# Kernel optimization log

Measured on AMD Instinct MI355X. Metric: run time of the kernel, lower is better.

The kernel has to match this reference:

```python
import jax, jax.numpy as jnp
import numpy as np

H_RES, W_RES = 32, 32
DIM = 512
NUM_HEADS = 16
HEAD_DIM = DIM // NUM_HEADS
SCALE = HEAD_DIM ** -0.5
B = 16
N = H_RES * W_RES
TABLE_SIZE = (2 * H_RES - 1) * (2 * W_RES - 1)


def _relative_position_index():
    coords_h = np.arange(H_RES)
    coords_w = np.arange(W_RES)
    coords = np.stack(np.meshgrid(coords_h, coords_w, indexing='ij'))  # [2, H, W]
    coords_flat = coords.reshape(2, -1)  # [2, N]
    rel = coords_flat[:, :, None] - coords_flat[:, None, :]  # [2, N, N]
    rel = rel.transpose(1, 2, 0).astype(np.int64)  # [N, N, 2]
    rel[:, :, 0] += H_RES - 1
    rel[:, :, 1] += W_RES - 1
    rel[:, :, 0] *= 2 * W_RES - 1
    return rel.sum(-1)  # [N, N]


def setup_inputs() -> dict:
    key = jax.random.key(0)
    ks = jax.random.split(key, 6)
    x = jax.random.normal(ks[0], (B, N, DIM), dtype=jnp.float32)
    w_qkv = jax.random.normal(ks[1], (DIM, 3 * DIM), dtype=jnp.float32) * (DIM ** -0.5)
    b_qkv = jnp.zeros((3 * DIM,), dtype=jnp.float32)
    w_proj = jax.random.normal(ks[2], (DIM, DIM), dtype=jnp.float32) * (DIM ** -0.5)
    b_proj = jnp.zeros((DIM,), dtype=jnp.float32)
    bias_table = jax.random.normal(ks[3], (TABLE_SIZE, NUM_HEADS), dtype=jnp.float32) * 0.02
    rel_index = jnp.asarray(_relative_position_index(), dtype=jnp.int32)
    return {"x": x, "w_qkv": w_qkv, "b_qkv": b_qkv, "w_proj": w_proj,
            "b_proj": b_proj, "bias_table": bias_table, "rel_index": rel_index}


def reference(x, w_qkv, b_qkv, w_proj, b_proj, bias_table, rel_index):
    Bq, Nq, C = x.shape
    qkv = x @ w_qkv + b_qkv  # [B, N, 3C]
    qkv = qkv.reshape(Bq, Nq, 3, NUM_HEADS, HEAD_DIM)
    q = qkv[:, :, 0].transpose(0, 2, 1, 3) * SCALE  # [B, nH, N, d]
    k = qkv[:, :, 1].transpose(0, 2, 1, 3)
    v = qkv[:, :, 2].transpose(0, 2, 1, 3)
    attn = jnp.einsum('bhnd,bhmd->bhnm', q, k)  # [B, nH, N, N]
    bias = bias_table[rel_index]  # [N, N, nH]
    attn = attn + bias.transpose(2, 0, 1)[None]  # broadcast over batch
    attn = jax.nn.softmax(attn, axis=-1)
    out = jnp.einsum('bhnm,bhmd->bhnd', attn, v)  # [B, nH, N, d]
    out = out.transpose(0, 2, 1, 3).reshape(Bq, Nq, C)
    return out @ w_proj + b_proj
```

## Files before the change

kernel.cpp:

```cpp
#include <hip/hip_runtime.h>
#include <hip/hip_bf16.h>
#include <cstdint>
#include <cstddef>

typedef _Float16 f16;
typedef __attribute__((ext_vector_type(8))) _Float16 f16x8;
typedef __attribute__((ext_vector_type(4))) _Float16 f16x4v;
typedef __bf16 bf16;
typedef __attribute__((ext_vector_type(4))) float f32x4;
typedef __attribute__((ext_vector_type(16))) float f32x16;

#define LOG2E 1.4426950408889634f
#define QK_SCALE 0.17677669529663687f

__device__ __forceinline__ f32x4 mfma16f(f16x8 a, f16x8 b, f32x4 c) {
  return __builtin_amdgcn_mfma_f32_16x16x32_f16(a, b, c, 0, 0, 0);
}
__device__ __forceinline__ f32x16 mfma32f(f16x8 a, f16x8 b, f32x16 c) {
  return __builtin_amdgcn_mfma_f32_32x32x16_f16(a, b, c, 0, 0, 0);
}
__device__ __forceinline__ float exp2_hw(float x) {
  float r; asm("v_exp_f32 %0, %1" : "=v"(r) : "v"(x)); return r;
}
__device__ __forceinline__ uint32_t cvtpk_f16(float a, float b) {
  uint32_t r; asm("v_cvt_pkrtz_f16_f32 %0, %1, %2" : "=v"(r) : "v"(a), "v"(b)); return r;
}
__device__ __forceinline__ void pl32swap(uint32_t& a, uint32_t& b) {
  asm("v_permlane32_swap_b32 %0, %1" : "+v"(a), "+v"(b));
}
__device__ __forceinline__ float lo16f(uint32_t u) { return __uint_as_float(u << 16); }
__device__ __forceinline__ float hi16f(uint32_t u) { return __uint_as_float(u & 0xFFFF0000u); }

__device__ __forceinline__ void gl16(const f16* g, f16* l) {
  __builtin_amdgcn_global_load_lds(
      (const __attribute__((address_space(1))) void*)g,
      (__attribute__((address_space(3))) void*)l, 16, 0, 0);
}

__device__ __forceinline__ uint32_t packoff(int m, int k) {
  return (((uint32_t)(m >> 7) * 16u + (uint32_t)(k >> 5)) * 8u + (uint32_t)((m >> 4) & 7)) * 512u
       + (uint32_t)((k >> 3) & 3) * 128u + (uint32_t)(m & 15) * 8u + (uint32_t)(k & 7);
}

__global__ __launch_bounds__(256) void prep_kernel(
    const float* __restrict__ x, const float* __restrict__ wqkv, const float* __restrict__ wproj,
    f16* __restrict__ Xp, f16* __restrict__ Wq, f16* __restrict__ Wp)
{
  const int X4 = 16384 * 512 / 4;
  int e = blockIdx.x * 256 + threadIdx.x;
  if (e < X4) {
    int m = e >> 7, k4 = e & 127;
    f32x4 v = *(const f32x4*)(x + (size_t)e * 4);
    f16x4v o;
    #pragma unroll
    for (int j = 0; j < 4; ++j) o[j] = (f16)v[j];
    *(f16x4v*)(Xp + packoff(m, k4 * 4)) = o;
  } else if (e < X4 + 1536 * 512) {
    int e2 = e - X4;
    int n = e2 >> 9, k = e2 & 511;
    Wq[packoff(n, k)] = (f16)wqkv[k * 1536 + n];
  } else {
    int e3 = e - (X4 + 1536 * 512);
    if (e3 < 512 * 512) {
      int n = e3 >> 9, k = e3 & 511;
      Wp[packoff(n, k)] = (f16)wproj[k * 512 + n];
    }
  }
}

__global__ __launch_bounds__(256) void tblT_kernel(
    const float* __restrict__ btab, float* __restrict__ tblT)
{
  int e = blockIdx.x * 256 + threadIdx.x;
  if (e < 3969 * 16) {
    int h = e & 15, i = e >> 4;
    tblT[h * 4000 + i] = btab[e] * LOG2E;
  }
}

__global__ __launch_bounds__(256) void biasC_kernel(
    const float* __restrict__ tblT, bf16* __restrict__ biasC)
{
  int t = blockIdx.x * 256 + threadIdx.x;
  if (t >= 16 * 63 * 64) return;
  int lane = t & 63;
  int sh = t >> 6;
  int s = sh % 63, h = sh / 63;
  int lq = lane & 31, hi5 = lane >> 5;
  const float* row = tblT + h * 4000 + s * 63 + 31 + lq;
  bf16 o[16];
  #pragma unroll
  for (int r = 0; r < 16; ++r) {
    int kx = (r & 3) + 8 * (r >> 2) + 4 * hi5;
    o[r] = (bf16)row[-kx];
  }
  *(uint4*)(biasC + (size_t)t * 16) = *(uint4*)&o[0];
  *(uint4*)(biasC + (size_t)t * 16 + 8) = *(uint4*)&o[8];
}

template<int NB>
__global__ __launch_bounds__(256) void gemm_frag(
    const f16* __restrict__ Ap, const f16* __restrict__ Bp,
    const float* __restrict__ bvec,
    f16* __restrict__ Qp, f16* __restrict__ Kp, f16* __restrict__ Vt,
    float* __restrict__ out)
{
  __shared__ f16 sA[3][4096];
  __shared__ f16 sB[3][4096];
  const int bid = blockIdx.x;
  const int xcd = bid & 7, idx = bid >> 3;
  int mb, nb;
  if (NB == 12) { int q = idx / 12; mb = xcd * 16 + q; nb = idx - q * 12; }
  else          { mb = xcd * 16 + (idx >> 2); nb = idx & 3; }
  const int tid = threadIdx.x, lane = tid & 63, wave = tid >> 6;
  const int l15 = lane & 15, l4 = lane >> 4;
  const int wr = wave >> 1, wc = wave & 1;

  const f16* gA = Ap + (uint32_t)mb * 65536u + (uint32_t)wave * 1024u + (uint32_t)lane * 8u;
  const f16* gB = Bp + (uint32_t)nb * 65536u + (uint32_t)wave * 1024u + (uint32_t)lane * 8u;
  const int wl = wave * 1024;

  gl16(gA,        &sA[0][wl]);
  gl16(gA + 512,  &sA[0][wl + 512]);
  gl16(gB,        &sB[0][wl]);
  gl16(gB + 512,  &sB[0][wl + 512]);
  gl16(gA + 4096, &sA[1][wl]);
  gl16(gA + 4608, &sA[1][wl + 512]);
  gl16(gB + 4096, &sB[1][wl]);
  gl16(gB + 4608, &sB[1][wl + 512]);

  f32x4 acc[4][4];
  #pragma unroll
  for (int i = 0; i < 4; ++i)
    #pragma unroll
    for (int j = 0; j < 4; ++j) acc[i][j] = (f32x4){0.f, 0.f, 0.f, 0.f};

  const uint32_t aoff = (uint32_t)(wr * 4) * 512u + (uint32_t)lane * 8u;
  const uint32_t boff = (uint32_t)(wc * 4) * 512u + (uint32_t)lane * 8u;

  #pragma unroll
  for (int kt = 0; kt < 16; ++kt) {
    const int s2 = (kt + 2) % 3;
    gl16(gA + (kt + 2) * 4096,       &sA[s2][wl]);
    gl16(gA + (kt + 2) * 4096 + 512, &sA[s2][wl + 512]);
    gl16(gB + (kt + 2) * 4096,       &sB[s2][wl]);
    gl16(gB + (kt + 2) * 4096 + 512, &sB[s2][wl + 512]);
    asm volatile("s_waitcnt vmcnt(8)" ::: "memory");
    asm volatile("s_barrier" ::: "memory");
    const int s0 = kt % 3;
    f16x8 af[4], bfr[4];
    #pragma unroll
    for (int f = 0; f < 4; ++f) {
      af[f]  = *(const f16x8*)&sA[s0][aoff + f * 512];
      bfr[f] = *(const f16x8*)&sB[s0][boff + f * 512];
    }
    asm volatile("s_waitcnt lgkmcnt(0)" ::: "memory");
    asm volatile("s_barrier" ::: "memory");
    #pragma unroll
    for (int mf = 0; mf < 4; ++mf)
      #pragma unroll
      for (int nf = 0; nf < 4; ++nf)
        acc[mf][nf] = mfma16f(af[mf], bfr[nf], acc[mf][nf]);
  }
  asm volatile("s_waitcnt vmcnt(0)" ::: "memory");

  #pragma unroll
  for (int mf = 0; mf < 4; ++mf) {
    #pragma unroll
    for (int nf = 0; nf < 4; ++nf) {
      int colb = nb * 128 + wc * 64 + nf * 16 + l15;
      float bb = bvec[colb];
      #pragma unroll
      for (int i = 0; i < 4; ++i) {
        int m = mb * 128 + wr * 64 + mf * 16 + l4 * 4 + i;
        float v = acc[mf][nf][i] + bb;
        if (NB == 4) {
          out[(size_t)m * 512 + colb] = v;
        } else {
          int t = colb >> 9, cc = colb & 511;
          int b = m >> 10, n = m & 1023;
          int hh = cc >> 5, d = cc & 31;
          int bh2 = b * 16 + hh;
          if (t == 0) {
            v *= (QK_SCALE * LOG2E);
            uint32_t off = (((uint32_t)bh2 * 32u + (uint32_t)(n >> 5)) * 2u + (uint32_t)(d >> 4)) * 512u
                         + ((uint32_t)((d >> 3) & 1) * 32u + (uint32_t)(n & 31)) * 8u + (uint32_t)(d & 7);
            Qp[off] = (f16)v;
          } else if (t == 1) {
            Kp[((size_t)(bh2 * 2 + (d >> 4)) * 1024 + n) * 16 + (d & 15)] = (f16)v;
          } else {
            Vt[((size_t)(bh2 * 128 + (n >> 3)) * 32 + d) * 8 + (n & 7)] = (f16)v;
          }
        }
      }
    }
  }
}

__global__ __launch_bounds__(256) void attn_kernel(
    const f16* __restrict__ Qp, const f16* __restrict__ Kp, const f16* __restrict__ Vt,
    const bf16* __restrict__ biasC, f16* __restrict__ Op)
{
  const int bid = blockIdx.x;
  const int xcd = bid & 7, slot = bid >> 3;
  const int h = xcd * 2 + (slot >> 6);
  const int rest = slot & 63;
  const int qg = rest >> 4, b = rest & 15;
  const int bh = b * 16 + h;
  const int tid = threadIdx.x, lane = tid & 63, wave = tid >> 6;
  const int lq = lane & 31, hi5 = lane >> 5;

  const int qb0 = qg * 8 + wave * 2;
  const int m0 = b * 1024 + qb0 * 32;

  const uint32_t qbase = ((uint32_t)bh * 32u + (uint32_t)qb0) * 1024u + (uint32_t)lane * 8u;
  const f16x8 q00 = *(const f16x8*)(Qp + qbase);
  const f16x8 q01 = *(const f16x8*)(Qp + qbase + 512);
  const f16x8 q10 = *(const f16x8*)(Qp + qbase + 1024);
  const f16x8 q11 = *(const f16x8*)(Qp + qbase + 1536);

  uint32_t koff = (uint32_t)bh * 32768u + (uint32_t)lq * 16u + (uint32_t)hi5 * 8u;
  uint32_t voff = (uint32_t)bh * 32768u + (uint32_t)hi5 * 256u + (uint32_t)lq * 8u;
  const bf16* bp = biasC + ((uint32_t)(h * 63 + qb0 + 31) * 64u + (uint32_t)lane) * 16u;

  f16x8 kA0 = *(const f16x8*)(Kp + koff);
  f16x8 kA1 = *(const f16x8*)(Kp + koff + 16384);
  uint4 p0A = *(const uint4*)(bp);
  uint4 p1A = *(const uint4*)(bp + 8);
  uint4 p2A = *(const uint4*)(bp + 1024);
  uint4 p3A = *(const uint4*)(bp + 1032);
  f16x8 vA0 = *(const f16x8*)(Vt + voff);
  f16x8 vA1 = *(const f16x8*)(Vt + voff + 512);
  f16x8 kB0 = *(const f16x8*)(Kp + koff + 512);
  f16x8 kB1 = *(const f16x8*)(Kp + koff + 16384 + 512);
  uint4 p0B = *(const uint4*)(bp - 1024);
  uint4 p1B = *(const uint4*)(bp - 1016);
  uint4 p2B = *(const uint4*)(bp);
  uint4 p3B = *(const uint4*)(bp + 8);
  f16x8 vB0 = *(const f16x8*)(Vt + voff + 1024);
  f16x8 vB1 = *(const f16x8*)(Vt + voff + 1536);

  f32x16 O0, O1, R0, R1;
  #pragma unroll
  for (int i = 0; i < 16; ++i) { O0[i] = 0.f; O1[i] = 0.f; R0[i] = 0.f; R1[i] = 0.f; }

  f16x8 onesv;
  { union { uint32_t u[4]; f16x8 v; } c;
    c.u[0] = c.u[1] = c.u[2] = c.u[3] = 0x3C003C00u; onesv = c.v; }

  union Uf { uint32_t u[4]; f16x8 v; };

#define UNPACK16(S, Pa, Pb)                              \
  S[0]  = lo16f(Pa.x); S[1]  = hi16f(Pa.x);              \
  S[2]  = lo16f(Pa.y); S[3]  = hi16f(Pa.y);              \
  S[4]  = lo16f(Pa.z); S[5]  = hi16f(Pa.z);              \
  S[6]  = lo16f(Pa.w); S[7]  = hi16f(Pa.w);              \
  S[8]  = lo16f(Pb.x); S[9]  = hi16f(Pb.x);              \
  S[10] = lo16f(Pb.y); S[11] = hi16f(Pb.y);              \
  S[12] = lo16f(Pb.z); S[13] = hi16f(Pb.z);              \
  S[14] = lo16f(Pb.w); S[15] = hi16f(Pb.w);

  auto tile = [&](f16x8& K0, f16x8& K1, f16x8& V0, f16x8& V1,
                  uint4& P0, uint4& P1, uint4& P2, uint4& P3,
                  uint32_t kpre, uint32_t vpre, int bpre) {
    asm volatile("s_waitcnt vmcnt(8)" ::: "memory");
    f32x16 S0, S1;
    UNPACK16(S0, P0, P1)
    UNPACK16(S1, P2, P3)
    S0 = mfma32f(K0, q00, S0);
    S0 = mfma32f(K1, q01, S0);
    S1 = mfma32f(K0, q10, S1);
    S1 = mfma32f(K1, q11, S1);
    K0 = *(const f16x8*)(Kp + koff + kpre);
    K1 = *(const f16x8*)(Kp + koff + 16384 + kpre);
    P0 = *(const uint4*)(bp + bpre);
    P1 = *(const uint4*)(bp + bpre + 8);
    P2 = *(const uint4*)(bp + bpre + 1024);
    P3 = *(const uint4*)(bp + bpre + 1032);
    __builtin_amdgcn_sched_barrier(0);
    {
      float e0  = exp2_hw(S0[0]),  e1  = exp2_hw(S0[1]),  e2  = exp2_hw(S0[2]),  e3  = exp2_hw(S0[3]);
      float e4  = exp2_hw(S0[4]),  e5  = exp2_hw(S0[5]),  e6  = exp2_hw(S0[6]),  e7  = exp2_hw(S0[7]);
      float e8  = exp2_hw(S0[8]),  e9  = exp2_hw(S0[9]),  e10 = exp2_hw(S0[10]), e11 = exp2_hw(S0[11]);
      float e12 = exp2_hw(S0[12]), e13 = exp2_hw(S0[13]), e14 = exp2_hw(S0[14]), e15 = exp2_hw(S0[15]);
      uint32_t u0 = cvtpk_f16(e0,  e1),  u1 = cvtpk_f16(e2,  e3);
      uint32_t u2 = cvtpk_f16(e4,  e5),  u3 = cvtpk_f16(e6,  e7);
      uint32_t u4 = cvtpk_f16(e8,  e9),  u5 = cvtpk_f16(e10, e11);
      uint32_t u6 = cvtpk_f16(e12, e13), u7 = cvtpk_f16(e14, e15);
      pl32swap(u0, u2); pl32swap(u1, u3); pl32swap(u4, u6); pl32swap(u5, u7);
      Uf a1; a1.u[0] = u0; a1.u[1] = u1; a1.u[2] = u2; a1.u[3] = u3;
      Uf a2; a2.u[0] = u4; a2.u[1] = u5; a2.u[2] = u6; a2.u[3] = u7;
      O0 = mfma32f(a1.v, V0, O0);
      O0 = mfma32f(a2.v, V1, O0);
      R0 = mfma32f(a1.v, onesv, R0);
      R0 = mfma32f(a2.v, onesv, R0);
    }
    {
      float e0  = exp2_hw(S1[0]),  e1  = exp2_hw(S1[1]),  e2  = exp2_hw(S1[2]),  e3  = exp2_hw(S1[3]);
      float e4  = exp2_hw(S1[4]),  e5  = exp2_hw(S1[5]),  e6  = exp2_hw(S1[6]),  e7  = exp2_hw(S1[7]);
      float e8  = exp2_hw(S1[8]),  e9  = exp2_hw(S1[9]),  e10 = exp2_hw(S1[10]), e11 = exp2_hw(S1[11]);
      float e12 = exp2_hw(S1[12]), e13 = exp2_hw(S1[13]), e14 = exp2_hw(S1[14]), e15 = exp2_hw(S1[15]);
      uint32_t u0 = cvtpk_f16(e0,  e1),  u1 = cvtpk_f16(e2,  e3);
      uint32_t u2 = cvtpk_f16(e4,  e5),  u3 = cvtpk_f16(e6,  e7);
      uint32_t u4 = cvtpk_f16(e8,  e9),  u5 = cvtpk_f16(e10, e11);
      uint32_t u6 = cvtpk_f16(e12, e13), u7 = cvtpk_f16(e14, e15);
      pl32swap(u0, u2); pl32swap(u1, u3); pl32swap(u4, u6); pl32swap(u5, u7);
      Uf a1; a1.u[0] = u0; a1.u[1] = u1; a1.u[2] = u2; a1.u[3] = u3;
      Uf a2; a2.u[0] = u4; a2.u[1] = u5; a2.u[2] = u6; a2.u[3] = u7;
      O1 = mfma32f(a1.v, V0, O1);
      O1 = mfma32f(a2.v, V1, O1);
      R1 = mfma32f(a1.v, onesv, R1);
      R1 = mfma32f(a2.v, onesv, R1);
    }
    V0 = *(const f16x8*)(Vt + voff + vpre);
    V1 = *(const f16x8*)(Vt + voff + vpre + 512);
    __builtin_amdgcn_sched_barrier(0);
  };

  #pragma unroll 1
  for (int it = 0; it < 16; ++it) {
    tile(kA0, kA1, vA0, vA1, p0A, p1A, p2A, p3A, 1024u, 2048u, -2048);
    tile(kB0, kB1, vB0, vB1, p0B, p1B, p2B, p3B, 1536u, 3072u, -3072);
    koff += 1024u; voff += 2048u; bp -= 2048;
  }

  const int kcol = h * 32 + lq;
  #pragma unroll
  for (int r = 0; r < 16; ++r) {
    int qrow = (r & 3) + 8 * (r >> 2) + 4 * hi5;
    Op[packoff(m0 + qrow, kcol)] = (f16)(O0[r] / R0[r]);
    Op[packoff(m0 + 32 + qrow, kcol)] = (f16)(O1[r] / R1[r]);
  }
}

extern "C" void kernel_launch(void* const* d_in, const int* in_sizes, int n_in,
                              void* d_out, int out_size, void* d_ws, size_t ws_size,
                              hipStream_t stream) {
  const float* x     = (const float*)d_in[0];
  const float* wqkv  = (const float*)d_in[1];
  const float* bqkv  = (const float*)d_in[2];
  const float* wproj = (const float*)d_in[3];
  const float* bproj = (const float*)d_in[4];
  const float* btab  = (const float*)d_in[5];
  float* out = (float*)d_out;

  char* ws = (char*)d_ws;
  size_t off = 0;
  auto walloc = [&](size_t bytes) {
    void* p = ws + off;
    off += (bytes + 255) & ~(size_t)255;
    return p;
  };
  const size_t PAD = 262144;
  f16* Xp   = (f16*)walloc((size_t)16384 * 512 * 2 + PAD);
  f16* Wq   = (f16*)walloc((size_t)1536 * 512 * 2 + PAD);
  f16* Wp   = (f16*)walloc((size_t)512 * 512 * 2 + PAD);
  float* tblT = (float*)walloc((size_t)16 * 4000 * 4);
  f16* Qp   = (f16*)walloc((size_t)16384 * 512 * 2 + PAD);
  f16* Kp   = (f16*)walloc((size_t)16384 * 512 * 2 + PAD);
  f16* Vt   = (f16*)walloc((size_t)16384 * 512 * 2 + PAD);
  bf16* biasC = (bf16*)walloc((size_t)16 * 63 * 64 * 16 * 2 + PAD);
  f16* Op   = (f16*)walloc((size_t)16384 * 512 * 2 + PAD);

  const int prep_total = 16384 * 512 / 4 + 1536 * 512 + 512 * 512;
  prep_kernel<<<(prep_total + 255) / 256, 256, 0, stream>>>(
      x, wqkv, wproj, Xp, Wq, Wp);

  tblT_kernel<<<(3969 * 16 + 255) / 256, 256, 0, stream>>>(btab, tblT);

  biasC_kernel<<<(16 * 63 * 64 + 255) / 256, 256, 0, stream>>>(tblT, biasC);

  gemm_frag<12><<<1536, 256, 0, stream>>>(
      Xp, Wq, bqkv, Qp, Kp, Vt, nullptr);

  attn_kernel<<<1024, 256, 0, stream>>>(Qp, Kp, Vt, biasC, Op);

  gemm_frag<4><<<512, 256, 0, stream>>>(
      Op, Wp, bproj, nullptr, nullptr, nullptr, out);
}
```

Baseline: 169.7 us.

## Replace ones-MFMA row sums with VALU accumulation and permute V layout

Drops the two extra MFMAs per half-tile that computed softmax row sums by multiplying with a ones vector, and instead accumulates the exp values in fp32 registers, reducing them with a cross-half shuffle at the end. It also removes the permlane32 swaps by permuting the key order inside the V layout written by the QKV GEMM epilogue, so the P fragment can be fed to the MFMA directly. Together these cut matrix-core work by roughly a third and remove the swap instructions, at the cost of extra VALU adds and a final shuffle per output row.

After: 160.7 us. 1.06x faster.

```diff
diff --git a/kernel.cpp b/kernel.cpp
--- a/kernel.cpp
+++ b/kernel.cpp
@@ -24,9 +24,6 @@
 }
 __device__ __forceinline__ uint32_t cvtpk_f16(float a, float b) {
   uint32_t r; asm("v_cvt_pkrtz_f16_f32 %0, %1, %2" : "=v"(r) : "v"(a), "v"(b)); return r;
-}
-__device__ __forceinline__ void pl32swap(uint32_t& a, uint32_t& b) {
-  asm("v_permlane32_swap_b32 %0, %1" : "+v"(a), "+v"(b));
 }
 __device__ __forceinline__ float lo16f(uint32_t u) { return __uint_as_float(u << 16); }
 __device__ __forceinline__ float hi16f(uint32_t u) { return __uint_as_float(u & 0xFFFF0000u); }
@@ -189,7 +186,10 @@
           } else if (t == 1) {
             Kp[((size_t)(bh2 * 2 + (d >> 4)) * 1024 + n) * 16 + (d & 15)] = (f16)v;
           } else {
-            Vt[((size_t)(bh2 * 128 + (n >> 3)) * 32 + d) * 8 + (n & 7)] = (f16)v;
+            int nl = n & 15;
+            int npl = (nl >= 4 && nl < 12) ? (nl ^ 12) : nl;
+            int np = (n & ~15) | npl;
+            Vt[((size_t)(bh2 * 128 + (np >> 3)) * 32 + d) * 8 + (np & 7)] = (f16)v;
           }
         }
       }
@@ -240,13 +240,10 @@
   f16x8 vB0 = *(const f16x8*)(Vt + voff + 1024);
   f16x8 vB1 = *(const f16x8*)(Vt + voff + 1536);
 
-  f32x16 O0, O1, R0, R1;
-  #pragma unroll
-  for (int i = 0; i < 16; ++i) { O0[i] = 0.f; O1[i] = 0.f; R0[i] = 0.f; R1[i] = 0.f; }
-
-  f16x8 onesv;
-  { union { uint32_t u[4]; f16x8 v; } c;
-    c.u[0] = c.u[1] = c.u[2] = c.u[3] = 0x3C003C00u; onesv = c.v; }
+  f32x16 O0, O1;
+  #pragma unroll
+  for (int i = 0; i < 16; ++i) { O0[i] = 0.f; O1[i] = 0.f; }
+  f32x4 racc0 = {0.f, 0.f, 0.f, 0.f}, racc1 = {0.f, 0.f, 0.f, 0.f};
 
   union Uf { uint32_t u[4]; f16x8 v; };
 
@@ -283,34 +280,34 @@
       float e4  = exp2_hw(S0[4]),  e5  = exp2_hw(S0[5]),  e6  = exp2_hw(S0[6]),  e7  = exp2_hw(S0[7]);
       float e8  = exp2_hw(S0[8]),  e9  = exp2_hw(S0[9]),  e10 = exp2_hw(S0[10]), e11 = exp2_hw(S0[11]);
       float e12 = exp2_hw(S0[12]), e13 = exp2_hw(S0[13]), e14 = exp2_hw(S0[14]), e15 = exp2_hw(S0[15]);
-      uint32_t u0 = cvtpk_f16(e0,  e1),  u1 = cvtpk_f16(e2,  e3);
-      uint32_t u2 = cvtpk_f16(e4,  e5),  u3 = cvtpk_f16(e6,  e7);
-      uint32_t u4 = cvtpk_f16(e8,  e9),  u5 = cvtpk_f16(e10, e11);
-      uint32_t u6 = cvtpk_f16(e12, e13), u7 = cvtpk_f16(e14, e15);
-      pl32swap(u0, u2); pl32swap(u1, u3); pl32swap(u4, u6); pl32swap(u5, u7);
-      Uf a1; a1.u[0] = u0; a1.u[1] = u1; a1.u[2] = u2; a1.u[3] = u3;
-      Uf a2; a2.u[0] = u4; a2.u[1] = u5; a2.u[2] = u6; a2.u[3] = u7;
+      racc0[0] += e0 + e4;   racc0[1] += e1 + e5;
+      racc0[2] += e2 + e6;   racc0[3] += e3 + e7;
+      racc0[0] += e8 + e12;  racc0[1] += e9 + e13;
+      racc0[2] += e10 + e14; racc0[3] += e11 + e15;
+      Uf a1, a2;
+      a1.u[0] = cvtpk_f16(e0,  e1);  a1.u[1] = cvtpk_f16(e2,  e3);
+      a1.u[2] = cvtpk_f16(e4,  e5);  a1.u[3] = cvtpk_f16(e6,  e7);
+      a2.u[0] = cvtpk_f16(e8,  e9);  a2.u[1] = cvtpk_f16(e10, e11);
+      a2.u[2] = cvtpk_f16(e12, e13); a2.u[3] = cvtpk_f16(e14, e15);
       O0 = mfma32f(a1.v, V0, O0);
       O0 = mfma32f(a2.v, V1, O0);
-      R0 = mfma32f(a1.v, onesv, R0);
-      R0 = mfma32f(a2.v, onesv, R0);
     }
     {
       float e0  = exp2_hw(S1[0]),  e1  = exp2_hw(S1[1]),  e2  = exp2_hw(S1[2]),  e3  = exp2_hw(S1[3]);
       float e4  = exp2_hw(S1[4]),  e5  = exp2_hw(S1[5]),  e6  = exp2_hw(S1[6]),  e7  = exp2_hw(S1[7]);
       float e8  = exp2_hw(S1[8]),  e9  = exp2_hw(S1[9]),  e10 = exp2_hw(S1[10]), e11 = exp2_hw(S1[11]);
       float e12 = exp2_hw(S1[12]), e13 = exp2_hw(S1[13]), e14 = exp2_hw(S1[14]), e15 = exp2_hw(S1[15]);
-      uint32_t u0 = cvtpk_f16(e0,  e1),  u1 = cvtpk_f16(e2,  e3);
-      uint32_t u2 = cvtpk_f16(e4,  e5),  u3 = cvtpk_f16(e6,  e7);
-      uint32_t u4 = cvtpk_f16(e8,  e9),  u5 = cvtpk_f16(e10, e11);
-      uint32_t u6 = cvtpk_f16(e12, e13), u7 = cvtpk_f16(e14, e15);
-      pl32swap(u0, u2); pl32swap(u1, u3); pl32swap(u4, u6); pl32swap(u5, u7);
-      Uf a1; a1.u[0] = u0; a1.u[1] = u1; a1.u[2] = u2; a1.u[3] = u3;
-      Uf a2; a2.u[0] = u4; a2.u[1] = u5; a2.u[2] = u6; a2.u[3] = u7;
+      racc1[0] += e0 + e4;   racc1[1] += e1 + e5;
+      racc1[2] += e2 + e6;   racc1[3] += e3 + e7;
+      racc1[0] += e8 + e12;  racc1[1] += e9 + e13;
+      racc1[2] += e10 + e14; racc1[3] += e11 + e15;
+      Uf a1, a2;
+      a1.u[0] = cvtpk_f16(e0,  e1);  a1.u[1] = cvtpk_f16(e2,  e3);
+      a1.u[2] = cvtpk_f16(e4,  e5);  a1.u[3] = cvtpk_f16(e6,  e7);
+      a2.u[0] = cvtpk_f16(e8,  e9);  a2.u[1] = cvtpk_f16(e10, e11);
+      a2.u[2] = cvtpk_f16(e12, e13); a2.u[3] = cvtpk_f16(e14, e15);
       O1 = mfma32f(a1.v, V0, O1);
       O1 = mfma32f(a2.v, V1, O1);
-      R1 = mfma32f(a1.v, onesv, R1);
-      R1 = mfma32f(a2.v, onesv, R1);
     }
     V0 = *(const f16x8*)(Vt + voff + vpre);
     V1 = *(const f16x8*)(Vt + voff + vpre + 512);
@@ -324,12 +321,21 @@
     koff += 1024u; voff += 2048u; bp -= 2048;
   }
 
+  float rs0 = (racc0[0] + racc0[1]) + (racc0[2] + racc0[3]);
+  rs0 += __shfl_xor(rs0, 32);
+  float inv0 = 1.0f / rs0;
+  float rs1 = (racc1[0] + racc1[1]) + (racc1[2] + racc1[3]);
+  rs1 += __shfl_xor(rs1, 32);
+  float inv1 = 1.0f / rs1;
+
   const int kcol = h * 32 + lq;
   #pragma unroll
   for (int r = 0; r < 16; ++r) {
     int qrow = (r & 3) + 8 * (r >> 2) + 4 * hi5;
-    Op[packoff(m0 + qrow, kcol)] = (f16)(O0[r] / R0[r]);
-    Op[packoff(m0 + 32 + qrow, kcol)] = (f16)(O1[r] / R1[r]);
+    float t0 = __shfl(inv0, qrow);
+    float t1 = __shfl(inv1, qrow);
+    Op[packoff(m0 + qrow, kcol)] = (f16)(O0[r] * t0);
+    Op[packoff(m0 + 32 + qrow, kcol)] = (f16)(O1[r] * t1);
   }
 }
 
```
